# Performance work log

Measured on AMD Instinct MI355X. Metric: run time of the kernel, lower is better.

## Reference

```python
import jax, jax.numpy as jnp
import numpy as np

NUM_HEADS = 8
BN_EPS = 1e-3


def _conv2d(x, w, padding):
    # x: (B, Cin, H, W), w: (Cout, Cin, kh, kw)
    return jax.lax.conv_general_dilated(
        x, w, window_strides=(1, 1), padding=padding,
        dimension_numbers=("NCHW", "OIHW", "NCHW"))


def setup_inputs() -> dict:
    key = jax.random.key(0)
    ks = jax.random.split(key, 6)
    B, C, H, W = 8, 256, 64, 64
    L, D = 80, 256
    return {
        "img_feat": jax.random.normal(ks[0], (B, C, H, W), jnp.float32),
        "text_feats": jax.random.normal(ks[1], (B, L, D), jnp.float32),
        "proj_w": jax.random.normal(ks[2], (D, C, 1, 1), jnp.float32) * (1.0 / np.sqrt(C)),
        "proj_b": jax.random.normal(ks[3], (D,), jnp.float32) * 0.02,
        "attn_bias": jnp.zeros((NUM_HEADS,), jnp.float32),
        "scale": jnp.ones((1, NUM_HEADS, 1, 1), jnp.float32),
        "conv_w": jax.random.normal(ks[4], (C, C, 3, 3), jnp.float32) * (1.0 / np.sqrt(9 * C)),
        "bn_gamma": jnp.ones((C,), jnp.float32),
        "bn_beta": jnp.zeros((C,), jnp.float32),
        "bn_mean": jnp.zeros((C,), jnp.float32),
        "bn_var": jnp.ones((C,), jnp.float32),
    }


def reference(img_feat, text_feats, proj_w, proj_b, attn_bias, scale,
              conv_w, bn_gamma, bn_beta, bn_mean, bn_var):
    B, C, H, W = img_feat.shape
    hc = proj_w.shape[0] // NUM_HEADS  # head_channels

    # img_proj: 1x1 conv + bias -> (B, heads, hc, H, W)
    i_feat = _conv2d(img_feat, proj_w, "VALID") + proj_b[None, :, None, None]
    i_feat = i_feat.reshape(B, NUM_HEADS, hc, H, W)

    # text: (B, L, heads, hc)
    t_feat = text_feats.reshape(B, -1, NUM_HEADS, hc)

    # attn score over text tokens, then max over tokens
    attn = jnp.einsum("bmchw,bnmc->bmhwn", i_feat, t_feat)  # (B, heads, H, W, L)
    attn = jnp.max(attn, axis=-1)
    attn = attn / jnp.sqrt(jnp.asarray(hc, img_feat.dtype))
    attn = attn + attn_bias[None, :, None, None]
    attn = jax.nn.sigmoid(attn) * scale  # (B, heads, H, W)

    # project_conv: 3x3 conv (no bias) + BN (inference), no activation
    x = _conv2d(img_feat, conv_w, [(1, 1), (1, 1)])
    inv = bn_gamma / jnp.sqrt(bn_var + BN_EPS)
    x = x * inv[None, :, None, None] + (bn_beta - bn_mean * inv)[None, :, None, None]

    # gate per head and flatten back to (B, C, H, W)
    x = x.reshape(B, NUM_HEADS, -1, H, W) * attn[:, :, None]
    return x.reshape(B, -1, H, W)
```

## Files before the change

### kernel.cpp

```cpp
#include <hip/hip_runtime.h>
#include <cmath>

constexpr int kB  = 8;
constexpr int kC  = 256;
constexpr int kH  = 64;
constexpr int kW  = 64;
constexpr int kP  = kH * kW;
constexpr int kL  = 80;
constexpr int kD  = 256;
constexpr int kNH = 8;

typedef short  short8 __attribute__((ext_vector_type(8)));
typedef float  f32x4  __attribute__((ext_vector_type(4)));
typedef unsigned short ushort_t;

__device__ __forceinline__ ushort_t f2bf(float f) {
  unsigned u = __builtin_bit_cast(unsigned, f);
  u += 0x7fffu + ((u >> 16) & 1u);
  return (ushort_t)(u >> 16);
}

__device__ __forceinline__ short8 pack8(float4 a, float4 b) {
  ushort_t tmp[8] = {f2bf(a.x), f2bf(a.y), f2bf(a.z), f2bf(a.w),
                     f2bf(b.x), f2bf(b.y), f2bf(b.z), f2bf(b.w)};
  return *(short8*)tmp;
}

__global__ __launch_bounds__(256) void transpose_img_kernel(
    const float* __restrict__ img, ushort_t* __restrict__ imgT) {
  __shared__ float Ls[64 * 67];
  const int b   = blockIdx.x;
  const int p0  = blockIdx.y * 64;
  const int ci0 = blockIdx.z * 64;
  const int t   = threadIdx.x;

  for (int e = t; e < 4096; e += 256) {
    int ci = e >> 6, px = e & 63;
    Ls[px * 67 + ci] = img[((size_t)(b * kC + ci0 + ci)) * kP + p0 + px];
  }
  __syncthreads();
  for (int u = t; u < 512; u += 256) {
    int px = u >> 3, cq = (u & 7) * 8;
    ushort_t tmp[8];
#pragma unroll
    for (int j = 0; j < 8; j++) tmp[j] = f2bf(Ls[px * 67 + cq + j]);
    *(uint4*)&imgT[((size_t)(b * kP + p0 + px)) * kC + ci0 + cq] = *(uint4*)tmp;
  }
}

__global__ __launch_bounds__(256) void prep_kernel(
    const float* __restrict__ cw, const float* __restrict__ pw,
    ushort_t* __restrict__ w2, ushort_t* __restrict__ pwb) {
  const int n_w2 = 9 * kC * kC;
  int idx = blockIdx.x * 256 + threadIdx.x;
  if (idx < n_w2) {
    int ci  = idx & 255;
    int co  = (idx >> 8) & 255;
    int tap = idx >> 16;
    w2[idx] = f2bf(cw[(co * kC + ci) * 9 + tap]);
  } else if (idx < n_w2 + kD * kC) {
    int r = idx - n_w2;
    pwb[r] = f2bf(pw[r]);
  }
}

__global__ __launch_bounds__(256) void attn_mfma_kernel(
    const ushort_t* __restrict__ imgT,
    const float* __restrict__ text,
    const ushort_t* __restrict__ pwb,
    const float* __restrict__ pb,
    const float* __restrict__ bias,
    const float* __restrict__ scale,
    float* __restrict__ attn_out) {
  __shared__ ushort_t SI[64 * 264];

  const int b    = blockIdx.x;
  const int p0   = blockIdx.y * 64;
  const int t    = threadIdx.x;
  const int w    = t >> 6;
  const int lane = t & 63;
  const int lr   = lane & 15;
  const int lq   = lane >> 4;
  const int d0   = w * 64;

  const ushort_t* imgTb = imgT + (size_t)b * kP * kC;

  f32x4 acc[4][4] = {};

  for (int kc = 0; kc < kC; kc += 32) {
    short8 afr[4], bfr[4];
#pragma unroll
    for (int mt = 0; mt < 4; mt++)
      afr[mt] = *(const short8*)&pwb[(size_t)(d0 + mt * 16 + lr) * kC + kc + lq * 8];
#pragma unroll
    for (int nt = 0; nt < 4; nt++)
      bfr[nt] = *(const short8*)&imgTb[(size_t)(p0 + nt * 16 + lr) * kC + kc + lq * 8];
#pragma unroll
    for (int mt = 0; mt < 4; mt++)
#pragma unroll
      for (int nt = 0; nt < 4; nt++)
        acc[mt][nt] = __builtin_amdgcn_mfma_f32_16x16x32_bf16(afr[mt], bfr[nt], acc[mt][nt], 0, 0, 0);
  }

#pragma unroll
  for (int mt = 0; mt < 4; mt++) {
    float4 pb4 = *(const float4*)(pb + d0 + mt * 16 + lq * 4);
#pragma unroll
    for (int nt = 0; nt < 4; nt++) {
      ushort_t v[4];
      v[0] = f2bf(acc[mt][nt][0] + pb4.x);
      v[1] = f2bf(acc[mt][nt][1] + pb4.y);
      v[2] = f2bf(acc[mt][nt][2] + pb4.z);
      v[3] = f2bf(acc[mt][nt][3] + pb4.w);
      *(ulonglong1*)&SI[(nt * 16 + lr) * 264 + d0 + mt * 16 + lq * 4] = *(ulonglong1*)v;
    }
  }

  const float* textb = text + (size_t)b * kL * kD;
#pragma unroll
  for (int lh = 0; lh < 2; lh++) {
    const int h = 2 * w + lh;
    const float bh = bias[h], sh = scale[h];
    short8 atok[5];
#pragma unroll
    for (int mt = 0; mt < 5; mt++) {
      const float* p = textb + (size_t)(mt * 16 + lr) * kD + h * 32 + lq * 8;
      atok[mt] = pack8(*(const float4*)p, *(const float4*)(p + 4));
    }
#pragma unroll
    for (int nt = 0; nt < 4; nt++) {
      short8 bfr2 = *(const short8*)&SI[(nt * 16 + lr) * 264 + h * 32 + lq * 8];
      float vmax = -3.4e38f;
#pragma unroll
      for (int mt = 0; mt < 5; mt++) {
        f32x4 z = {};
        f32x4 d = __builtin_amdgcn_mfma_f32_16x16x32_bf16(atok[mt], bfr2, z, 0, 0, 0);
        vmax = fmaxf(vmax, fmaxf(fmaxf(d[0], d[1]), fmaxf(d[2], d[3])));
      }
      vmax = fmaxf(vmax, __shfl_xor(vmax, 16));
      vmax = fmaxf(vmax, __shfl_xor(vmax, 32));
      if (lq == 0) {
        float lg = vmax * 0.17677669529663687f + bh;
        float a  = sh / (1.0f + expf(-lg));
        attn_out[((size_t)(b * kNH + h)) * kP + p0 + nt * 16 + lr] = a;
      }
    }
  }
}

__global__ __launch_bounds__(256) void conv_mfma_kernel(
    const ushort_t* __restrict__ imgT,
    const ushort_t* __restrict__ w2,
    const float* __restrict__ gamma,
    const float* __restrict__ beta,
    const float* __restrict__ mean,
    const float* __restrict__ var,
    const float* __restrict__ attn,
    float* __restrict__ out) {
  __shared__ ushort_t Al[6 * 66 * 40];
  __shared__ ushort_t Wl[9 * 64 * 40];

  const int b   = blockIdx.x;
  const int h0  = blockIdx.y * 4;
  const int co0 = blockIdx.z * 64;
  const int t   = threadIdx.x;
  const int w   = t >> 6;
  const int lane = t & 63;
  const int lr  = lane & 15;
  const int lq  = lane >> 4;

  const ushort_t* imgTb = imgT + (size_t)b * kP * kC;

  f32x4 acc[4][4] = {};

  for (int kc = 0; kc < kC; kc += 32) {
    __syncthreads();
    for (int e = t; e < 6 * 66 * 4; e += 256) {
      int r   = e / 264;
      int rem = e - r * 264;
      int c   = rem >> 2;
      int cq  = (rem & 3) * 8;
      int row = h0 - 1 + r;
      uint4 v = make_uint4(0, 0, 0, 0);
      if (row >= 0 && row < kH && c >= 1 && c <= 64) {
        int px = row * kW + (c - 1);
        v = *(const uint4*)&imgTb[(size_t)px * kC + kc + cq];
      }
      *(uint4*)&Al[(r * 66 + c) * 40 + cq] = v;
    }
    {
      int e = t;
#pragma unroll
      for (int i = 0; i < 9; i++, e += 256) {
        int cq  = (e & 3) * 8;
        int co  = (e >> 2) & 63;
        int tap = e >> 8;
        uint4 v = *(const uint4*)&w2[((size_t)(tap * kC + co0 + co)) * kC + kc + cq];
        *(uint4*)&Wl[(tap * 64 + co) * 40 + cq] = v;
      }
    }
    __syncthreads();

    const int abase = (w * 66 + lr) * 40 + lq * 8;
    const int wbase = lr * 40 + lq * 8;
#pragma unroll
    for (int tap = 0; tap < 9; tap++) {
      const int kh = tap / 3, kw = tap % 3;
      short8 bi[4];
#pragma unroll
      for (int nt = 0; nt < 4; nt++)
        bi[nt] = *(const short8*)&Al[abase + (kh * 66 + kw + nt * 16) * 40];
      short8 aw[4];
#pragma unroll
      for (int mt = 0; mt < 4; mt++)
        aw[mt] = *(const short8*)&Wl[wbase + (tap * 64 + mt * 16) * 40];
#pragma unroll
      for (int mt = 0; mt < 4; mt++)
#pragma unroll
        for (int nt = 0; nt < 4; nt++)
          acc[mt][nt] = __builtin_amdgcn_mfma_f32_16x16x32_bf16(
              aw[mt], bi[nt], acc[mt][nt], 0, 0, 0);
    }
  }

  const int h = h0 + w;
  float* outb = out + (size_t)b * kC * kP + h * kW;
#pragma unroll
  for (int mt = 0; mt < 4; mt++) {
    const int head = (co0 + mt * 16) >> 5;
    const float* arow = attn + ((size_t)(b * kNH + head)) * kP + h * kW;
    float inv_v[4], bb_v[4];
#pragma unroll
    for (int reg = 0; reg < 4; reg++) {
      int co = co0 + mt * 16 + lq * 4 + reg;
      float inv = gamma[co] * rsqrtf(var[co] + 1e-3f);
      inv_v[reg] = inv;
      bb_v[reg]  = beta[co] - mean[co] * inv;
    }
#pragma unroll
    for (int nt = 0; nt < 4; nt++) {
      const int col = nt * 16 + lr;
      const float av = arow[col];
#pragma unroll
      for (int reg = 0; reg < 4; reg++) {
        int co = co0 + mt * 16 + lq * 4 + reg;
        outb[(size_t)co * kP + col] = (acc[mt][nt][reg] * inv_v[reg] + bb_v[reg]) * av;
      }
    }
  }
}

extern "C" void kernel_launch(void* const* d_in, const int* in_sizes, int n_in,
                              void* d_out, int out_size, void* d_ws, size_t ws_size,
                              hipStream_t stream) {
  const float* img   = (const float*)d_in[0];
  const float* text  = (const float*)d_in[1];
  const float* pw    = (const float*)d_in[2];
  const float* pb    = (const float*)d_in[3];
  const float* bias  = (const float*)d_in[4];
  const float* scale = (const float*)d_in[5];
  const float* cw    = (const float*)d_in[6];
  const float* gam   = (const float*)d_in[7];
  const float* bet   = (const float*)d_in[8];
  const float* mea   = (const float*)d_in[9];
  const float* va    = (const float*)d_in[10];
  float* out = (float*)d_out;

  char* ws = (char*)d_ws;
  float*    attn = (float*)ws;
  ushort_t* imgT = (ushort_t*)(ws + (1u << 20));
  ushort_t* w2   = (ushort_t*)(ws + (1u << 20) + (16u << 20));
  ushort_t* pwb  = (ushort_t*)(ws + (1u << 20) + (16u << 20) + 1179648u);

  {
    dim3 grid(kB, kP / 64, kC / 64);
    transpose_img_kernel<<<grid, 256, 0, stream>>>(img, imgT);
  }
  {
    int n = 9 * kC * kC + kD * kC;
    prep_kernel<<<(n + 255) / 256, 256, 0, stream>>>(cw, pw, w2, pwb);
  }
  {
    dim3 grid(kB, kP / 64);
    attn_mfma_kernel<<<grid, 256, 0, stream>>>(imgT, text, pwb, pb, bias, scale, attn);
  }
  {
    dim3 grid(kB, kH / 4, kC / 64);
    conv_mfma_kernel<<<grid, 256, 0, stream>>>(imgT, w2, gam, bet, mea, va, attn, out);
  }
}
```

Measured before the change: 174.3 us.

## Fuse image transpose/bf16 conversion into attention projection kernel

Removes the separate transpose kernel and has the attention kernel read fp32 NCHW image data, convert it to bf16 into a shared-memory tile, feed the MFMA B operand from LDS, and write the transposed imgT for the later conv kernel. This saves a kernel launch and a global re-read of imgT by the attention kernel. In exchange it adds two barriers per K step, and the global loads of the fp32 image are only 64 floats contiguous per row, which may reduce load efficiency.

```diff
diff --git a/kernel.cpp b/kernel.cpp
--- a/kernel.cpp
+++ b/kernel.cpp
@@ -24,28 +24,6 @@
   ushort_t tmp[8] = {f2bf(a.x), f2bf(a.y), f2bf(a.z), f2bf(a.w),
                      f2bf(b.x), f2bf(b.y), f2bf(b.z), f2bf(b.w)};
   return *(short8*)tmp;
-}
-
-__global__ __launch_bounds__(256) void transpose_img_kernel(
-    const float* __restrict__ img, ushort_t* __restrict__ imgT) {
-  __shared__ float Ls[64 * 67];
-  const int b   = blockIdx.x;
-  const int p0  = blockIdx.y * 64;
-  const int ci0 = blockIdx.z * 64;
-  const int t   = threadIdx.x;
-
-  for (int e = t; e < 4096; e += 256) {
-    int ci = e >> 6, px = e & 63;
-    Ls[px * 67 + ci] = img[((size_t)(b * kC + ci0 + ci)) * kP + p0 + px];
-  }
-  __syncthreads();
-  for (int u = t; u < 512; u += 256) {
-    int px = u >> 3, cq = (u & 7) * 8;
-    ushort_t tmp[8];
-#pragma unroll
-    for (int j = 0; j < 8; j++) tmp[j] = f2bf(Ls[px * 67 + cq + j]);
-    *(uint4*)&imgT[((size_t)(b * kP + p0 + px)) * kC + ci0 + cq] = *(uint4*)tmp;
-  }
 }
 
 __global__ __launch_bounds__(256) void prep_kernel(
@@ -65,13 +43,15 @@
 }
 
 __global__ __launch_bounds__(256) void attn_mfma_kernel(
-    const ushort_t* __restrict__ imgT,
+    const float* __restrict__ img,
     const float* __restrict__ text,
     const ushort_t* __restrict__ pwb,
     const float* __restrict__ pb,
     const float* __restrict__ bias,
     const float* __restrict__ scale,
+    ushort_t* __restrict__ imgT,
     float* __restrict__ attn_out) {
+  __shared__ ushort_t SB[64 * 40];
   __shared__ ushort_t SI[64 * 264];
 
   const int b    = blockIdx.x;
@@ -83,18 +63,34 @@
   const int lq   = lane >> 4;
   const int d0   = w * 64;
 
-  const ushort_t* imgTb = imgT + (size_t)b * kP * kC;
+  const float* imgb  = img  + (size_t)b * kC * kP + p0;
+  ushort_t*    imgTb = imgT + (size_t)(b * kP + p0) * kC;
 
   f32x4 acc[4][4] = {};
 
   for (int kc = 0; kc < kC; kc += 32) {
+    __syncthreads();
+#pragma unroll
+    for (int i = 0; i < 4; i++) {
+      int e = t + i * 256;
+      int px = e & 63, ci2 = (e >> 6) * 2;
+      ushort_t u[2];
+      u[0] = f2bf(imgb[(size_t)(kc + ci2)     * kP + px]);
+      u[1] = f2bf(imgb[(size_t)(kc + ci2 + 1) * kP + px]);
+      *(unsigned*)&SB[px * 40 + ci2] = *(unsigned*)u;
+    }
+    __syncthreads();
+    {
+      int px = t >> 2, cq = (t & 3) * 8;
+      *(uint4*)&imgTb[(size_t)px * kC + kc + cq] = *(const uint4*)&SB[px * 40 + cq];
+    }
     short8 afr[4], bfr[4];
 #pragma unroll
     for (int mt = 0; mt < 4; mt++)
       afr[mt] = *(const short8*)&pwb[(size_t)(d0 + mt * 16 + lr) * kC + kc + lq * 8];
 #pragma unroll
     for (int nt = 0; nt < 4; nt++)
-      bfr[nt] = *(const short8*)&imgTb[(size_t)(p0 + nt * 16 + lr) * kC + kc + lq * 8];
+      bfr[nt] = *(const short8*)&SB[(nt * 16 + lr) * 40 + lq * 8];
 #pragma unroll
     for (int mt = 0; mt < 4; mt++)
 #pragma unroll
@@ -273,16 +269,12 @@
   ushort_t* pwb  = (ushort_t*)(ws + (1u << 20) + (16u << 20) + 1179648u);
 
   {
-    dim3 grid(kB, kP / 64, kC / 64);
-    transpose_img_kernel<<<grid, 256, 0, stream>>>(img, imgT);
-  }
-  {
     int n = 9 * kC * kC + kD * kC;
     prep_kernel<<<(n + 255) / 256, 256, 0, stream>>>(cw, pw, w2, pwb);
   }
   {
     dim3 grid(kB, kP / 64);
-    attn_mfma_kernel<<<grid, 256, 0, stream>>>(imgT, text, pwb, pb, bias, scale, attn);
+    attn_mfma_kernel<<<grid, 256, 0, stream>>>(img, text, pwb, pb, bias, scale, imgT, attn);
   }
   {
     dim3 grid(kB, kH / 4, kC / 64);
```

Result: faster. 159.5 us (-8.5%).
